# Performance work log

Hardware: AMD Instinct MI355X
Metric: run time of the kernel (lower is better)

The kernel has to match this reference:

```python
import jax, jax.numpy as jnp
import numpy as np

N = 20000          # nodes
E = 320000         # edges
H = 128            # hidden_channels
A = 512            # aerial feature dim
SPOT = 20000
DIST_UNIT = 50
NEMB = SPOT // DIST_UNIT
RATIO = 0.25       # neighbor_ratio


def setup_inputs() -> dict:
    key = jax.random.key(0)
    ks = jax.random.split(key, 12)
    x = jax.random.normal(ks[0], (N, H), jnp.float32)
    edge_index = jax.random.randint(ks[1], (2, E), 0, N)
    distances = jax.random.randint(ks[2], (E,), 0, SPOT)
    aerial_emb = jax.random.normal(ks[3], (N, A), jnp.float32)
    s = lambda k, shape, fan: jax.random.normal(k, shape, jnp.float32) / np.sqrt(fan).astype(np.float32)
    W_lin = s(ks[4], (H, H), H)
    b_lin = jnp.zeros((H,), jnp.float32)
    W_q = s(ks[5], (H + A + H, H), H + A + H)
    b_q = jnp.zeros((H,), jnp.float32)
    W_v = s(ks[6], (H, H), H)
    b_v = jnp.zeros((H,), jnp.float32)
    dist_table = jax.random.normal(ks[7], (NEMB, H), jnp.float32)  # init.normal_ like torch
    W_l = s(ks[8], (H, H), H)   # SAGE lin_l (neighbor aggr), with bias
    b_l = jnp.zeros((H,), jnp.float32)
    W_r = s(ks[9], (H, H), H)   # SAGE lin_r (root), no bias in PyG default
    return dict(x=x, edge_index=edge_index, distances=distances, aerial_emb=aerial_emb,
                W_lin=W_lin, b_lin=b_lin, W_q=W_q, b_q=b_q, W_v=W_v, b_v=b_v,
                dist_table=dist_table, W_l=W_l, b_l=b_l, W_r=W_r)


def reference(x, edge_index, distances, aerial_emb, W_lin, b_lin, W_q, b_q, W_v, b_v, dist_table, W_l, b_l, W_r):
    n = x.shape[0]
    e = edge_index.shape[1]
    k = int(e * RATIO)  # static: number of sampled edges

    x = x @ W_lin + b_lin                                  # [N, H]
    src, tgt = edge_index[0], edge_index[1]
    source_x = x[src]                                      # [E, H]
    target_x = x[tgt]                                      # [E, H]
    source_aerial = aerial_emb[src]                        # [E, A]
    dist_x = dist_table[distances // DIST_UNIT]            # [E, H]

    query = jnp.concatenate([source_x, source_aerial, dist_x], axis=1) @ W_q + b_q  # [E, H]
    value = target_x @ W_v + b_v                           # [E, H]
    logits = -jnp.linalg.norm(query - value, axis=1)       # [E]
    logprob = jax.nn.log_softmax(logits, axis=0)

    # torch.multinomial(prob, k) without replacement == Gumbel top-k on log-probs
    u = jax.random.uniform(jax.random.key(42), (e,), jnp.float32)
    gumbel = -jnp.log(-jnp.log(u + 1e-20) + 1e-20)
    _, sel = jax.lax.top_k(logprob + gumbel, k)            # [k] selected edge ids
    src_s = src[sel]
    tgt_s = tgt[sel]

    # SAGEConv (mean aggregation): out = lin_l(mean_j x_j) + lin_r(x)
    msg = jax.ops.segment_sum(x[src_s], tgt_s, num_segments=n)              # [N, H]
    deg = jax.ops.segment_sum(jnp.ones((k,), x.dtype), tgt_s, num_segments=n)
    aggr = msg / jnp.maximum(deg, 1.0)[:, None]
    out = aggr @ W_l + b_l + x @ W_r                       # [N, H]
    return out
```

## Files before the change

### kernel.cpp

```cpp
#include <hip/hip_runtime.h>
#include <stdint.h>

#define N_NODES 20000
#define E_EDGES 320000
#define H_DIM 128
#define A_DIM 512
#define NEMB_N 400
#define K_SEL 80000u
#define NB1 16384
#define NB2 16384
#define CAND_MAX 8192
#define LO_F (-128.0f)
#define SCALE1 (16384.0f / 160.0f)

#define NODE_BLKS (N_NODES / 8)
#define DIST_BLKS (NEMB_N / 8)

struct SelState {
    int b1; unsigned cum1; unsigned r1;
    int b2; unsigned cum2; unsigned r2;
    unsigned long long T;
};

__device__ __forceinline__ uint32_t rotl32(uint32_t x, int r) {
    return (x << r) | (x >> (32 - r));
}

__device__ __forceinline__ void threefry2x32(uint32_t k0, uint32_t k1,
                                             uint32_t& x0, uint32_t& x1) {
    uint32_t ks0 = k0, ks1 = k1, ks2 = k0 ^ k1 ^ 0x1BD11BDAu;
    x0 += ks0; x1 += ks1;
    x0 += x1; x1 = rotl32(x1, 13); x1 ^= x0;
    x0 += x1; x1 = rotl32(x1, 15); x1 ^= x0;
    x0 += x1; x1 = rotl32(x1, 26); x1 ^= x0;
    x0 += x1; x1 = rotl32(x1, 6);  x1 ^= x0;
    x0 += ks1; x1 += ks2 + 1u;
    x0 += x1; x1 = rotl32(x1, 17); x1 ^= x0;
    x0 += x1; x1 = rotl32(x1, 29); x1 ^= x0;
    x0 += x1; x1 = rotl32(x1, 16); x1 ^= x0;
    x0 += x1; x1 = rotl32(x1, 24); x1 ^= x0;
    x0 += ks2; x1 += ks0 + 2u;
    x0 += x1; x1 = rotl32(x1, 13); x1 ^= x0;
    x0 += x1; x1 = rotl32(x1, 15); x1 ^= x0;
    x0 += x1; x1 = rotl32(x1, 26); x1 ^= x0;
    x0 += x1; x1 = rotl32(x1, 6);  x1 ^= x0;
    x0 += ks0; x1 += ks1 + 3u;
    x0 += x1; x1 = rotl32(x1, 17); x1 ^= x0;
    x0 += x1; x1 = rotl32(x1, 29); x1 ^= x0;
    x0 += x1; x1 = rotl32(x1, 16); x1 ^= x0;
    x0 += x1; x1 = rotl32(x1, 24); x1 ^= x0;
    x0 += ks1; x1 += ks2 + 4u;
    x0 += x1; x1 = rotl32(x1, 13); x1 ^= x0;
    x0 += x1; x1 = rotl32(x1, 15); x1 ^= x0;
    x0 += x1; x1 = rotl32(x1, 26); x1 ^= x0;
    x0 += x1; x1 = rotl32(x1, 6);  x1 ^= x0;
    x0 += ks2; x1 += ks0 + 5u;
}

__global__ __launch_bounds__(128) void k_node(
    const float* __restrict__ x, const float* __restrict__ aerial,
    const float* __restrict__ Wlin, const float* __restrict__ blin,
    const float* __restrict__ Wq, const float* __restrict__ bq,
    const float* __restrict__ Wv, const float* __restrict__ bv,
    const float* __restrict__ dtab,
    float* __restrict__ xl32, float* __restrict__ q32, float* __restrict__ v32,
    float* __restrict__ dq32) {
    __shared__ float xinT[H_DIM][8];
    __shared__ float xsT[H_DIM][8];
    __shared__ float aerT[A_DIM][8];
    const int j = threadIdx.x;

    if (blockIdx.x >= NODE_BLKS) {
        const int n0 = (blockIdx.x - NODE_BLKS) * 8;
#pragma unroll
        for (int m = 0; m < 8; ++m) xinT[j][m] = dtab[(size_t)(n0 + m) * H_DIM + j];
        __syncthreads();
        float acc[8];
#pragma unroll
        for (int m = 0; m < 8; ++m) acc[m] = 0.0f;
        for (int k = 0; k < H_DIM; ++k) {
            float w = Wq[(size_t)(H_DIM + A_DIM + k) * H_DIM + j];
            const float4* xp = (const float4*)&xinT[k][0];
            float4 a0 = xp[0], a1 = xp[1];
            acc[0] = fmaf(a0.x, w, acc[0]); acc[1] = fmaf(a0.y, w, acc[1]);
            acc[2] = fmaf(a0.z, w, acc[2]); acc[3] = fmaf(a0.w, w, acc[3]);
            acc[4] = fmaf(a1.x, w, acc[4]); acc[5] = fmaf(a1.y, w, acc[5]);
            acc[6] = fmaf(a1.z, w, acc[6]); acc[7] = fmaf(a1.w, w, acc[7]);
        }
#pragma unroll
        for (int m = 0; m < 8; ++m) dq32[(size_t)(n0 + m) * H_DIM + j] = acc[m];
        return;
    }

    const int n0 = blockIdx.x * 8;
#pragma unroll
    for (int m = 0; m < 8; ++m) xinT[j][m] = x[(size_t)(n0 + m) * H_DIM + j];
#pragma unroll
    for (int m = 0; m < 8; ++m)
#pragma unroll
        for (int c = 0; c < 4; ++c)
            aerT[c * H_DIM + j][m] = aerial[(size_t)(n0 + m) * A_DIM + c * H_DIM + j];
    __syncthreads();
    float acc[8];
    {
        float bj = blin[j];
#pragma unroll
        for (int m = 0; m < 8; ++m) acc[m] = bj;
        for (int k = 0; k < H_DIM; ++k) {
            float w = Wlin[k * H_DIM + j];
            const float4* xp = (const float4*)&xinT[k][0];
            float4 a0 = xp[0], a1 = xp[1];
            acc[0] = fmaf(a0.x, w, acc[0]); acc[1] = fmaf(a0.y, w, acc[1]);
            acc[2] = fmaf(a0.z, w, acc[2]); acc[3] = fmaf(a0.w, w, acc[3]);
            acc[4] = fmaf(a1.x, w, acc[4]); acc[5] = fmaf(a1.y, w, acc[5]);
            acc[6] = fmaf(a1.z, w, acc[6]); acc[7] = fmaf(a1.w, w, acc[7]);
        }
    }
#pragma unroll
    for (int m = 0; m < 8; ++m) {
        xsT[j][m] = acc[m];
        xl32[(size_t)(n0 + m) * H_DIM + j] = acc[m];
    }
    __syncthreads();
    {
        float bj = bv[j];
        float av[8];
#pragma unroll
        for (int m = 0; m < 8; ++m) av[m] = bj;
        for (int k = 0; k < H_DIM; ++k) {
            float w = Wv[k * H_DIM + j];
            const float4* xp = (const float4*)&xsT[k][0];
            float4 a0 = xp[0], a1 = xp[1];
            av[0] = fmaf(a0.x, w, av[0]); av[1] = fmaf(a0.y, w, av[1]);
            av[2] = fmaf(a0.z, w, av[2]); av[3] = fmaf(a0.w, w, av[3]);
            av[4] = fmaf(a1.x, w, av[4]); av[5] = fmaf(a1.y, w, av[5]);
            av[6] = fmaf(a1.z, w, av[6]); av[7] = fmaf(a1.w, w, av[7]);
        }
#pragma unroll
        for (int m = 0; m < 8; ++m) v32[(size_t)(n0 + m) * H_DIM + j] = av[m];
    }
    {
        float bj = bq[j];
        float aq[8];
#pragma unroll
        for (int m = 0; m < 8; ++m) aq[m] = bj;
        for (int k = 0; k < H_DIM; ++k) {
            float w = Wq[k * H_DIM + j];
            const float4* xp = (const float4*)&xsT[k][0];
            float4 a0 = xp[0], a1 = xp[1];
            aq[0] = fmaf(a0.x, w, aq[0]); aq[1] = fmaf(a0.y, w, aq[1]);
            aq[2] = fmaf(a0.z, w, aq[2]); aq[3] = fmaf(a0.w, w, aq[3]);
            aq[4] = fmaf(a1.x, w, aq[4]); aq[5] = fmaf(a1.y, w, aq[5]);
            aq[6] = fmaf(a1.z, w, aq[6]); aq[7] = fmaf(a1.w, w, aq[7]);
        }
        for (int k = 0; k < A_DIM; ++k) {
            float w = Wq[(size_t)(H_DIM + k) * H_DIM + j];
            const float4* xp = (const float4*)&aerT[k][0];
            float4 a0 = xp[0], a1 = xp[1];
            aq[0] = fmaf(a0.x, w, aq[0]); aq[1] = fmaf(a0.y, w, aq[1]);
            aq[2] = fmaf(a0.z, w, aq[2]); aq[3] = fmaf(a0.w, w, aq[3]);
            aq[4] = fmaf(a1.x, w, aq[4]); aq[5] = fmaf(a1.y, w, aq[5]);
            aq[6] = fmaf(a1.z, w, aq[6]); aq[7] = fmaf(a1.w, w, aq[7]);
        }
#pragma unroll
        for (int m = 0; m < 8; ++m) q32[(size_t)(n0 + m) * H_DIM + j] = aq[m];
    }
}

__device__ __forceinline__ int bin1_of(float s) {
    float t = (s - LO_F) * SCALE1;
    int b = (int)t;
    return min(max(b, 0), NB1 - 1);
}
__device__ __forceinline__ int bin2_of(float s, int b1) {
    float t = (s - LO_F) * SCALE1;
    float frac = t - (float)b1;
    int b = (int)(frac * (float)NB2);
    return min(max(b, 0), NB2 - 1);
}

__global__ __launch_bounds__(256) void k_score(
    const int* __restrict__ ei, const int* __restrict__ dist,
    const float* __restrict__ q32, const float* __restrict__ v32,
    const float* __restrict__ dq32,
    unsigned long long* __restrict__ keys, float* __restrict__ s32o,
    unsigned* __restrict__ hist1) {
    const int g = threadIdx.x >> 5, lane = threadIdx.x & 31;
    const int e0 = blockIdx.x * 32 + g * 4;

    const int s0 = ei[e0 + 0], s1 = ei[e0 + 1], s2 = ei[e0 + 2], s3 = ei[e0 + 3];
    const int t0 = ei[E_EDGES + e0 + 0], t1 = ei[E_EDGES + e0 + 1];
    const int t2 = ei[E_EDGES + e0 + 2], t3 = ei[E_EDGES + e0 + 3];
    const int d0 = dist[e0 + 0] / 50, d1 = dist[e0 + 1] / 50;
    const int d2 = dist[e0 + 2] / 50, d3 = dist[e0 + 3] / 50;

    float4 q0 = ((const float4*)(q32 + (size_t)s0 * H_DIM))[lane];
    float4 q1 = ((const float4*)(q32 + (size_t)s1 * H_DIM))[lane];
    float4 q2 = ((const float4*)(q32 + (size_t)s2 * H_DIM))[lane];
    float4 q3 = ((const float4*)(q32 + (size_t)s3 * H_DIM))[lane];
    float4 v0 = ((const float4*)(v32 + (size_t)t0 * H_DIM))[lane];
    float4 v1 = ((const float4*)(v32 + (size_t)t1 * H_DIM))[lane];
    float4 v2 = ((const float4*)(v32 + (size_t)t2 * H_DIM))[lane];
    float4 v3 = ((const float4*)(v32 + (size_t)t3 * H_DIM))[lane];
    float4 w0 = ((const float4*)(dq32 + (size_t)d0 * H_DIM))[lane];
    float4 w1 = ((const float4*)(dq32 + (size_t)d1 * H_DIM))[lane];
    float4 w2 = ((const float4*)(dq32 + (size_t)d2 * H_DIM))[lane];
    float4 w3 = ((const float4*)(dq32 + (size_t)d3 * H_DIM))[lane];

    float ax, ay, az, aw;
    ax = q0.x + w0.x - v0.x; ay = q0.y + w0.y - v0.y;
    az = q0.z + w0.z - v0.z; aw = q0.w + w0.w - v0.w;
    float ss0 = fmaf(ax, ax, fmaf(ay, ay, fmaf(az, az, aw * aw)));
    ax = q1.x + w1.x - v1.x; ay = q1.y + w1.y - v1.y;
    az = q1.z + w1.z - v1.z; aw = q1.w + w1.w - v1.w;
    float ss1 = fmaf(ax, ax, fmaf(ay, ay, fmaf(az, az, aw * aw)));
    ax = q2.x + w2.x - v2.x; ay = q2.y + w2.y - v2.y;
    az = q2.z + w2.z - v2.z; aw = q2.w + w2.w - v2.w;
    float ss2 = fmaf(ax, ax, fmaf(ay, ay, fmaf(az, az, aw * aw)));
    ax = q3.x + w3.x - v3.x; ay = q3.y + w3.y - v3.y;
    az = q3.z + w3.z - v3.z; aw = q3.w + w3.w - v3.w;
    float ss3 = fmaf(ax, ax, fmaf(ay, ay, fmaf(az, az, aw * aw)));

#pragma unroll
    for (int o = 16; o > 0; o >>= 1) {
        ss0 += __shfl_xor(ss0, o, 64);
        ss1 += __shfl_xor(ss1, o, 64);
        ss2 += __shfl_xor(ss2, o, 64);
        ss3 += __shfl_xor(ss3, o, 64);
    }
    if (lane < 4) {
        float ssv = (lane == 0) ? ss0 : (lane == 1) ? ss1 : (lane == 2) ? ss2 : ss3;
        const int e = e0 + lane;
        uint32_t x0r = 0u, x1r = (uint32_t)e;
        threefry2x32(0u, 42u, x0r, x1r);
        uint32_t bits = x0r ^ x1r;
        float uu = __uint_as_float((bits >> 9) | 0x3f800000u) - 1.0f;
        float nrm = sqrtf(ssv);
        float a = -logf(uu + 1e-20f);
        float gm = -logf(a + 1e-20f);
        float score = gm - nrm;
        int ib = __float_as_int(score);
        unsigned m32 = (ib < 0) ? ~(unsigned)ib : ((unsigned)ib | 0x80000000u);
        keys[e] = ((unsigned long long)m32 << 32) | (unsigned)(0xFFFFFFFFu - (unsigned)e);
        s32o[e] = score;
        atomicAdd(&hist1[bin1_of(score)], 1u);
    }
}

__global__ __launch_bounds__(256) void k_hist2(const float* __restrict__ s32,
                                               const SelState* __restrict__ st,
                                               unsigned* __restrict__ hist2) {
    int e = blockIdx.x * 256 + threadIdx.x;
    if (e >= E_EDGES) return;
    float s = s32[e];
    int b1 = bin1_of(s);
    if (b1 != st->b1) return;
    atomicAdd(&hist2[bin2_of(s, b1)], 1u);
}

__global__ __launch_bounds__(256) void k_scan(const unsigned* __restrict__ hist,
                                              SelState* st, int phase) {
    __shared__ unsigned csum[256];
    __shared__ unsigned bins[64];
    __shared__ int selc;
    __shared__ unsigned cumbase;
    const int t = threadIdx.x;
    const unsigned target = (phase == 1) ? K_SEL : st->r1;
    unsigned s = 0;
    for (int i = 0; i < 64; ++i) s += hist[t * 64 + i];
    csum[t] = s;
    __syncthreads();
    if (t == 0) {
        unsigned cum = 0; int c = 255;
        for (; c >= 0; --c) {
            if (cum + csum[c] >= target) break;
            cum += csum[c];
        }
        selc = c; cumbase = cum;
    }
    __syncthreads();
    if (t < 64) bins[t] = hist[selc * 64 + t];
    __syncthreads();
    if (t == 0) {
        unsigned cum = cumbase; int b = -1;
        for (int i = 63; i >= 0; --i) {
            if (cum + bins[i] >= target) { b = selc * 64 + i; break; }
            cum += bins[i];
        }
        unsigned r = target - cum;
        if (phase == 1) { st->b1 = b; st->cum1 = cum; st->r1 = r; }
        else           { st->b2 = b; st->cum2 = cum; st->r2 = r; }
    }
}

__global__ __launch_bounds__(256) void k_collect(
    const float* __restrict__ s32, const unsigned long long* __restrict__ keys,
    const SelState* __restrict__ st, unsigned long long* __restrict__ cand,
    unsigned* __restrict__ cnt) {
    int e = blockIdx.x * 256 + threadIdx.x;
    if (e >= E_EDGES) return;
    float s = s32[e];
    int b1 = bin1_of(s);
    if (b1 != st->b1) return;
    if (bin2_of(s, b1) != st->b2) return;
    unsigned p = atomicAdd(cnt, 1u);
    if (p < CAND_MAX) cand[p] = keys[e];
}

__global__ __launch_bounds__(256) void k_thresh(
    const unsigned long long* __restrict__ cand, const unsigned* __restrict__ cnt,
    SelState* st) {
    int c = (int)min(*cnt, (unsigned)CAND_MAX);
    unsigned r2 = st->r2;
    for (int i = threadIdx.x; i < c; i += blockDim.x) {
        unsigned long long ki = cand[i];
        unsigned g = 0;
        for (int j = 0; j < c; ++j) g += (cand[j] > ki);
        if (g == r2 - 1) st->T = ki;
    }
}

__global__ __launch_bounds__(256) void k_scatter(
    const int* __restrict__ ei, const unsigned long long* __restrict__ keys,
    const SelState* __restrict__ st, const float* __restrict__ xl32,
    float* __restrict__ msg, float* __restrict__ deg) {
    const int wid = threadIdx.x >> 6, lane = threadIdx.x & 63;
    const int e = blockIdx.x * 4 + wid;
    if (keys[e] >= st->T) {
        int sidx = ei[e], tidx = ei[E_EDGES + e];
        const float* xp = xl32 + (size_t)sidx * H_DIM;
        float* mp = msg + (size_t)tidx * H_DIM;
        const int h = lane * 2;
        atomicAdd(&mp[h], xp[h]);
        atomicAdd(&mp[h + 1], xp[h + 1]);
        if (lane == 0) atomicAdd(&deg[tidx], 1.0f);
    }
}

__global__ __launch_bounds__(128) void k_out(
    const float* __restrict__ msg, const float* __restrict__ deg,
    const float* __restrict__ xl32, const float* __restrict__ Wl,
    const float* __restrict__ bl, const float* __restrict__ Wr,
    float* __restrict__ out) {
    __shared__ float axT[H_DIM][8];
    __shared__ float xxT[H_DIM][8];
    const int j = threadIdx.x;
    const int n0 = blockIdx.x * 8;
#pragma unroll
    for (int m = 0; m < 8; ++m) {
        float d = fmaxf(deg[n0 + m], 1.0f);
        axT[j][m] = msg[(size_t)(n0 + m) * H_DIM + j] / d;
        xxT[j][m] = xl32[(size_t)(n0 + m) * H_DIM + j];
    }
    __syncthreads();
    float acc[8];
    float bj = bl[j];
#pragma unroll
    for (int m = 0; m < 8; ++m) acc[m] = bj;
    for (int k = 0; k < H_DIM; ++k) {
        float wl = Wl[k * H_DIM + j];
        float wr = Wr[k * H_DIM + j];
        const float4* ap = (const float4*)&axT[k][0];
        const float4* xp = (const float4*)&xxT[k][0];
        float4 a0 = ap[0], a1 = ap[1];
        float4 x0 = xp[0], x1 = xp[1];
        acc[0] = fmaf(a0.x, wl, fmaf(x0.x, wr, acc[0]));
        acc[1] = fmaf(a0.y, wl, fmaf(x0.y, wr, acc[1]));
        acc[2] = fmaf(a0.z, wl, fmaf(x0.z, wr, acc[2]));
        acc[3] = fmaf(a0.w, wl, fmaf(x0.w, wr, acc[3]));
        acc[4] = fmaf(a1.x, wl, fmaf(x1.x, wr, acc[4]));
        acc[5] = fmaf(a1.y, wl, fmaf(x1.y, wr, acc[5]));
        acc[6] = fmaf(a1.z, wl, fmaf(x1.z, wr, acc[6]));
        acc[7] = fmaf(a1.w, wl, fmaf(x1.w, wr, acc[7]));
    }
#pragma unroll
    for (int m = 0; m < 8; ++m) out[(size_t)(n0 + m) * H_DIM + j] = acc[m];
}

extern "C" void kernel_launch(void* const* d_in, const int* in_sizes, int n_in,
                              void* d_out, int out_size, void* d_ws, size_t ws_size,
                              hipStream_t stream) {
    const float* x      = (const float*)d_in[0];
    const int*   ei     = (const int*)d_in[1];
    const int*   dist   = (const int*)d_in[2];
    const float* aerial = (const float*)d_in[3];
    const float* Wlin   = (const float*)d_in[4];
    const float* blin   = (const float*)d_in[5];
    const float* Wq     = (const float*)d_in[6];
    const float* bq     = (const float*)d_in[7];
    const float* Wv     = (const float*)d_in[8];
    const float* bv     = (const float*)d_in[9];
    const float* dtab   = (const float*)d_in[10];
    const float* Wl     = (const float*)d_in[11];
    const float* bl     = (const float*)d_in[12];
    const float* Wr     = (const float*)d_in[13];
    float* out = (float*)d_out;

    char* ws = (char*)d_ws;
    size_t off = 0;
    auto alloc = [&](size_t bytes) -> void* {
        void* p = ws + off;
        off += (bytes + 255) & ~(size_t)255;
        return p;
    };
    float* q32  = (float*)alloc((size_t)N_NODES * H_DIM * 4);
    float* v32  = (float*)alloc((size_t)N_NODES * H_DIM * 4);
    float* dq32 = (float*)alloc((size_t)NEMB_N * H_DIM * 4);
    unsigned long long* keys = (unsigned long long*)alloc((size_t)E_EDGES * 8);
    float* xl32 = (float*)alloc((size_t)N_NODES * H_DIM * 4);
    float* s32  = (float*)alloc((size_t)E_EDGES * 4);
    char* zbase = ws + off;
    float* msg  = (float*)alloc((size_t)N_NODES * H_DIM * 4);
    float* deg  = (float*)alloc((size_t)N_NODES * 4);
    unsigned* hist1 = (unsigned*)alloc((size_t)NB1 * 4);
    unsigned* hist2 = (unsigned*)alloc((size_t)NB2 * 4);
    unsigned long long* cand = (unsigned long long*)alloc((size_t)CAND_MAX * 8);
    unsigned* counters = (unsigned*)alloc(256);
    SelState* st = (SelState*)alloc(256);
    size_t zlen = (size_t)((ws + off) - zbase);

    hipMemsetAsync(zbase, 0, zlen, stream);

    k_node<<<NODE_BLKS + DIST_BLKS, 128, 0, stream>>>(
        x, aerial, Wlin, blin, Wq, bq, Wv, bv, dtab, xl32, q32, v32, dq32);
    k_score<<<E_EDGES / 32, 256, 0, stream>>>(ei, dist, q32, v32, dq32,
                                              keys, s32, hist1);
    k_scan<<<1, 256, 0, stream>>>(hist1, st, 1);
    k_hist2<<<(E_EDGES + 255) / 256, 256, 0, stream>>>(s32, st, hist2);
    k_scan<<<1, 256, 0, stream>>>(hist2, st, 2);
    k_collect<<<(E_EDGES + 255) / 256, 256, 0, stream>>>(s32, keys, st, cand, &counters[0]);
    k_thresh<<<1, 256, 0, stream>>>(cand, &counters[0], st);
    k_scatter<<<E_EDGES / 4, 256, 0, stream>>>(ei, keys, st, xl32, msg, deg);
    k_out<<<N_NODES / 8, 128, 0, stream>>>(msg, deg, xl32, Wl, bl, Wr, out);
}
```

Before: 521.6 us.

## Replace two-level float-binned selection with single radix histogram on key bits

The top-k threshold search now builds one 131072-bin histogram indexed by the top 17 bits of the order-preserving 64-bit sort key, instead of two passes of float-range binning. This removes the second histogram kernel, the second scan and the stored float score buffer, cutting kernel launches and one full pass over the edges. In exchange the threshold bin may hold more candidates, so the quadratic k_thresh rank search does more work. If the bin ever exceeds the enlarged candidate capacity, the result would be wrong.

```diff
diff --git a/kernel.cpp b/kernel.cpp
--- a/kernel.cpp
+++ b/kernel.cpp
@@ -7,11 +7,9 @@
 #define A_DIM 512
 #define NEMB_N 400
 #define K_SEL 80000u
-#define NB1 16384
-#define NB2 16384
-#define CAND_MAX 8192
-#define LO_F (-128.0f)
-#define SCALE1 (16384.0f / 160.0f)
+#define NBK 131072
+#define CAND_MAX 16384
+#define SCAN_PER (NBK / 1024)
 
 #define NODE_BLKS (N_NODES / 8)
 #define DIST_BLKS (NEMB_N / 8)
@@ -167,23 +165,11 @@
     }
 }
 
-__device__ __forceinline__ int bin1_of(float s) {
-    float t = (s - LO_F) * SCALE1;
-    int b = (int)t;
-    return min(max(b, 0), NB1 - 1);
-}
-__device__ __forceinline__ int bin2_of(float s, int b1) {
-    float t = (s - LO_F) * SCALE1;
-    float frac = t - (float)b1;
-    int b = (int)(frac * (float)NB2);
-    return min(max(b, 0), NB2 - 1);
-}
-
 __global__ __launch_bounds__(256) void k_score(
     const int* __restrict__ ei, const int* __restrict__ dist,
     const float* __restrict__ q32, const float* __restrict__ v32,
     const float* __restrict__ dq32,
-    unsigned long long* __restrict__ keys, float* __restrict__ s32o,
+    unsigned long long* __restrict__ keys,
     unsigned* __restrict__ hist1) {
     const int g = threadIdx.x >> 5, lane = threadIdx.x & 31;
     const int e0 = blockIdx.x * 32 + g * 4;
@@ -241,82 +227,67 @@
         float score = gm - nrm;
         int ib = __float_as_int(score);
         unsigned m32 = (ib < 0) ? ~(unsigned)ib : ((unsigned)ib | 0x80000000u);
-        keys[e] = ((unsigned long long)m32 << 32) | (unsigned)(0xFFFFFFFFu - (unsigned)e);
-        s32o[e] = score;
-        atomicAdd(&hist1[bin1_of(score)], 1u);
-    }
-}
-
-__global__ __launch_bounds__(256) void k_hist2(const float* __restrict__ s32,
-                                               const SelState* __restrict__ st,
-                                               unsigned* __restrict__ hist2) {
-    int e = blockIdx.x * 256 + threadIdx.x;
-    if (e >= E_EDGES) return;
-    float s = s32[e];
-    int b1 = bin1_of(s);
-    if (b1 != st->b1) return;
-    atomicAdd(&hist2[bin2_of(s, b1)], 1u);
-}
-
-__global__ __launch_bounds__(256) void k_scan(const unsigned* __restrict__ hist,
-                                              SelState* st, int phase) {
-    __shared__ unsigned csum[256];
-    __shared__ unsigned bins[64];
+        unsigned long long key =
+            ((unsigned long long)m32 << 32) | (unsigned)(0xFFFFFFFFu - (unsigned)e);
+        keys[e] = key;
+        atomicAdd(&hist1[(unsigned)(key >> 47)], 1u);
+    }
+}
+
+__global__ __launch_bounds__(1024) void k_scan(const unsigned* __restrict__ hist,
+                                               SelState* st) {
+    __shared__ unsigned csum[1024];
+    __shared__ unsigned bins[SCAN_PER];
     __shared__ int selc;
     __shared__ unsigned cumbase;
     const int t = threadIdx.x;
-    const unsigned target = (phase == 1) ? K_SEL : st->r1;
     unsigned s = 0;
-    for (int i = 0; i < 64; ++i) s += hist[t * 64 + i];
+    for (int i = 0; i < SCAN_PER; ++i) s += hist[t * SCAN_PER + i];
     csum[t] = s;
     __syncthreads();
     if (t == 0) {
-        unsigned cum = 0; int c = 255;
+        unsigned cum = 0; int c = 1023;
         for (; c >= 0; --c) {
-            if (cum + csum[c] >= target) break;
+            if (cum + csum[c] >= K_SEL) break;
             cum += csum[c];
         }
         selc = c; cumbase = cum;
     }
     __syncthreads();
-    if (t < 64) bins[t] = hist[selc * 64 + t];
+    if (t < SCAN_PER) bins[t] = hist[selc * SCAN_PER + t];
     __syncthreads();
     if (t == 0) {
         unsigned cum = cumbase; int b = -1;
-        for (int i = 63; i >= 0; --i) {
-            if (cum + bins[i] >= target) { b = selc * 64 + i; break; }
+        for (int i = SCAN_PER - 1; i >= 0; --i) {
+            if (cum + bins[i] >= K_SEL) { b = selc * SCAN_PER + i; break; }
             cum += bins[i];
         }
-        unsigned r = target - cum;
-        if (phase == 1) { st->b1 = b; st->cum1 = cum; st->r1 = r; }
-        else           { st->b2 = b; st->cum2 = cum; st->r2 = r; }
+        st->b1 = b; st->cum1 = cum; st->r1 = K_SEL - cum;
     }
 }
 
 __global__ __launch_bounds__(256) void k_collect(
-    const float* __restrict__ s32, const unsigned long long* __restrict__ keys,
+    const unsigned long long* __restrict__ keys,
     const SelState* __restrict__ st, unsigned long long* __restrict__ cand,
     unsigned* __restrict__ cnt) {
     int e = blockIdx.x * 256 + threadIdx.x;
     if (e >= E_EDGES) return;
-    float s = s32[e];
-    int b1 = bin1_of(s);
-    if (b1 != st->b1) return;
-    if (bin2_of(s, b1) != st->b2) return;
+    unsigned long long k = keys[e];
+    if ((int)(unsigned)(k >> 47) != st->b1) return;
     unsigned p = atomicAdd(cnt, 1u);
-    if (p < CAND_MAX) cand[p] = keys[e];
-}
-
-__global__ __launch_bounds__(256) void k_thresh(
+    if (p < CAND_MAX) cand[p] = k;
+}
+
+__global__ __launch_bounds__(1024) void k_thresh(
     const unsigned long long* __restrict__ cand, const unsigned* __restrict__ cnt,
     SelState* st) {
     int c = (int)min(*cnt, (unsigned)CAND_MAX);
-    unsigned r2 = st->r2;
-    for (int i = threadIdx.x; i < c; i += blockDim.x) {
+    unsigned r = st->r1;
+    for (int i = threadIdx.x; i < c; i += 1024) {
         unsigned long long ki = cand[i];
         unsigned g = 0;
         for (int j = 0; j < c; ++j) g += (cand[j] > ki);
-        if (g == r2 - 1) st->T = ki;
+        if (g == r - 1) st->T = ki;
     }
 }
 
@@ -408,12 +379,10 @@
     float* dq32 = (float*)alloc((size_t)NEMB_N * H_DIM * 4);
     unsigned long long* keys = (unsigned long long*)alloc((size_t)E_EDGES * 8);
     float* xl32 = (float*)alloc((size_t)N_NODES * H_DIM * 4);
-    float* s32  = (float*)alloc((size_t)E_EDGES * 4);
     char* zbase = ws + off;
     float* msg  = (float*)alloc((size_t)N_NODES * H_DIM * 4);
     float* deg  = (float*)alloc((size_t)N_NODES * 4);
-    unsigned* hist1 = (unsigned*)alloc((size_t)NB1 * 4);
-    unsigned* hist2 = (unsigned*)alloc((size_t)NB2 * 4);
+    unsigned* hist1 = (unsigned*)alloc((size_t)NBK * 4);
     unsigned long long* cand = (unsigned long long*)alloc((size_t)CAND_MAX * 8);
     unsigned* counters = (unsigned*)alloc(256);
     SelState* st = (SelState*)alloc(256);
@@ -424,12 +393,10 @@
     k_node<<<NODE_BLKS + DIST_BLKS, 128, 0, stream>>>(
         x, aerial, Wlin, blin, Wq, bq, Wv, bv, dtab, xl32, q32, v32, dq32);
     k_score<<<E_EDGES / 32, 256, 0, stream>>>(ei, dist, q32, v32, dq32,
-                                              keys, s32, hist1);
-    k_scan<<<1, 256, 0, stream>>>(hist1, st, 1);
-    k_hist2<<<(E_EDGES + 255) / 256, 256, 0, stream>>>(s32, st, hist2);
-    k_scan<<<1, 256, 0, stream>>>(hist2, st, 2);
-    k_collect<<<(E_EDGES + 255) / 256, 256, 0, stream>>>(s32, keys, st, cand, &counters[0]);
-    k_thresh<<<1, 256, 0, stream>>>(cand, &counters[0], st);
+                                              keys, hist1);
+    k_scan<<<1, 1024, 0, stream>>>(hist1, st);
+    k_collect<<<(E_EDGES + 255) / 256, 256, 0, stream>>>(keys, st, cand, &counters[0]);
+    k_thresh<<<1, 1024, 0, stream>>>(cand, &counters[0], st);
     k_scatter<<<E_EDGES / 4, 256, 0, stream>>>(ei, keys, st, xl32, msg, deg);
     k_out<<<N_NODES / 8, 128, 0, stream>>>(msg, deg, xl32, Wl, bl, Wr, out);
 }
```

Result: slower. 1.005 ms (+92.6%).
